# Kernel optimization log

Hardware: AMD Instinct MI355X
Metric: run time of the kernel (lower is better)

## Reference

```python
import jax, jax.numpy as jnp
import numpy as np

B, T, C = 4, 1536, 1536
H, DK, DV = 8, 64, 192
NB = 32  # num_basis per feature class: 192 // (2*3)
MIN_HALF_LIFE = 3.0


def pos_feats_all(distances, seq_len, nb=NB):
    """Enformer positional basis: [exponential, central_mask, gamma], asymmetric.
    distances: int array [L]; returns [L, 6*nb] float32."""
    pos = jnp.abs(distances).astype(jnp.float32)[:, None]  # [L,1]
    sl = jnp.float32(seq_len)
    # exponential
    max_range = jnp.log(sl) / jnp.log(2.0)
    half_life = jnp.power(2.0, jnp.linspace(MIN_HALF_LIFE, max_range, nb))  # [nb]
    f_exp = jnp.exp(-jnp.log(2.0) / half_life * pos)
    # central mask
    widths = jnp.power(2.0, jnp.arange(1, nb + 1, dtype=jnp.float32)) - 1.0
    f_cm = (widths > pos).astype(jnp.float32)
    # gamma
    stddev = sl / (2.0 * nb)
    start_mean = sl / nb
    mean = jnp.linspace(start_mean, sl, nb)
    conc = (mean / stddev) ** 2
    rate = mean / stddev ** 2
    log_unnorm = (conc - 1.0) * jnp.log(pos) - rate * pos  # log(0)=-inf -> exp=0 at pos=0
    log_norm = jax.lax.lgamma(conc) - conc * jnp.log(rate)
    prob = jnp.exp(log_unnorm - log_norm) + 1e-8
    f_gm = prob / jnp.max(prob, axis=0, keepdims=True)
    emb = jnp.concatenate([f_exp, f_cm, f_gm], axis=-1)  # [L, 3*nb]
    sign = jnp.sign(distances).astype(jnp.float32)[:, None]
    return jnp.concatenate([emb, sign * emb], axis=-1)  # [L, 6*nb]


def relative_shift(x):
    """x: [B,H,T,2T-1] -> [B,H,T,T] via the Transformer-XL shift trick."""
    b, h, t, l = x.shape  # l = 2t-1
    x = jnp.pad(x, ((0, 0), (0, 0), (0, 0), (1, 0)))  # [b,h,t,2t]
    x = x.reshape(b, h, l + 1, t)[:, :, 1:, :].reshape(b, h, t, l)
    return x[..., :t]


def setup_inputs() -> dict:
    key = jax.random.key(0)
    ks = jax.random.split(key, 10)
    def dense(k, fi, fo):  # VarianceScaling(scale=2.0)-like init
        return (jax.random.normal(k, (fi, fo), jnp.float32) * np.sqrt(2.0 / fi)).astype(jnp.float32)
    return {
        "x": jax.random.normal(ks[0], (B, T, C), jnp.float32),
        "W_q": dense(ks[1], C, H * DK),
        "W_k": dense(ks[2], C, H * DK),
        "W_v": dense(ks[3], C, H * DV),
        "W_rel_k": dense(ks[4], 6 * NB, H * DK),
        "W_out": dense(ks[5], H * DV, H * DV),
        "b_out": jnp.zeros((H * DV,), jnp.float32),
        "r_w_bias": jax.random.normal(ks[6], (1, H, 1, DK), jnp.float32) * np.sqrt(2.0 / DK),
        "r_r_bias": jax.random.normal(ks[7], (1, H, 1, DK), jnp.float32) * np.sqrt(2.0 / DK),
    }


def reference(x, W_q, W_k, W_v, W_rel_k, W_out, b_out, r_w_bias, r_r_bias):
    b, t, _ = x.shape
    def heads(w, d):  # [b,t,H*d] -> [b,H,t,d]
        return (x @ w).reshape(b, t, H, d).transpose(0, 2, 1, 3)
    Q = heads(W_q, DK) * (DK ** -0.5)  # scaling applied before biases
    K = heads(W_k, DK)
    V = heads(W_v, DV)
    distances = jnp.arange(-t + 1, t)  # [2t-1]
    pe = pos_feats_all(distances, t)  # [2t-1, 6*NB]
    rK = (pe @ W_rel_k).reshape(2 * t - 1, H, DK).transpose(1, 0, 2)  # [H, 2t-1, DK]
    content = jnp.einsum('bhqd,bhkd->bhqk', Q + r_w_bias, K)
    rel = jnp.einsum('bhqd,hld->bhql', Q + r_r_bias, rK)  # [b,H,t,2t-1]
    logits = content + relative_shift(rel)
    attn = jax.nn.softmax(logits, axis=-1)
    out = jnp.einsum('bhqk,bhkd->bhqd', attn, V)  # [b,H,t,DV]
    out = out.transpose(0, 2, 1, 3).reshape(b, t, H * DV)
    return out @ W_out + b_out
```

## Files before the change

kernel.cpp:

```cpp
#include <hip/hip_runtime.h>
#include <hip/hip_bf16.h>
#include <math.h>

#define BB 4
#define TT 1536
#define CC 1536
#define HH 8
#define DKk 64
#define DVv 192
#define NBASIS 32
#define LREL 3071
#define MROWS 6144

typedef short short8 __attribute__((ext_vector_type(8)));
typedef float floatx4 __attribute__((ext_vector_type(4)));

static __device__ inline short f2bf(float f) {
  __hip_bfloat16 h = __float2bfloat16(f);
  return *reinterpret_cast<short*>(&h);
}

static __device__ inline void gload_lds16(const __hip_bfloat16* g, __hip_bfloat16* l) {
  __builtin_amdgcn_global_load_lds(
      (const __attribute__((address_space(1))) unsigned int*)g,
      (__attribute__((address_space(3))) unsigned int*)l, 16, 0, 0);
}

__global__ void detect_kernel(const void* __restrict__ x, int* __restrict__ flag) {
  if (threadIdx.x == 0 && blockIdx.x == 0) {
    const __hip_bfloat16* h = (const __hip_bfloat16*)x;
    int cnt = 0;
    for (int i = 0; i < 64; ++i) {
      float v = fabsf((float)h[2 * i]);
      if (v > 1e-5f && v < 256.0f) cnt++;
    }
    *flag = (cnt >= 32) ? 1 : 0;
  }
}

__global__ __launch_bounds__(256) void convert_kernel(const void* __restrict__ src,
                                                      float* __restrict__ dst, int n,
                                                      const int* __restrict__ flag) {
  const int i = blockIdx.x * 256 + threadIdx.x;
  if (i >= n) return;
  if (*flag) dst[i] = (float)((const __hip_bfloat16*)src)[i];
  else       dst[i] = ((const float*)src)[i];
}

__global__ __launch_bounds__(256) void convbf_kernel(const void* __restrict__ src,
                                                     __hip_bfloat16* __restrict__ dst, int n,
                                                     const int* __restrict__ flag) {
  const int i = blockIdx.x * 256 + threadIdx.x;
  if (i >= n) return;
  if (*flag) dst[i] = ((const __hip_bfloat16*)src)[i];
  else       dst[i] = __float2bfloat16(((const float*)src)[i]);
}

__global__ __launch_bounds__(256) void wt_kernel(const void* __restrict__ src,
                                                 __hip_bfloat16* __restrict__ dst,
                                                 int K, int N, const int* __restrict__ flag) {
  __shared__ __hip_bfloat16 tile[64][68];
  const int tid = threadIdx.x;
  const int k0 = blockIdx.y * 64, n0 = blockIdx.x * 64;
  const bool bf = (*flag != 0);
  {
    const int r = tid >> 2, c0 = (tid & 3) * 16;
    if (bf) {
      const __hip_bfloat16* sp = (const __hip_bfloat16*)src + (size_t)(k0 + r) * N + n0 + c0;
#pragma unroll
      for (int u = 0; u < 16; ++u) tile[r][c0 + u] = sp[u];
    } else {
      const float* sp = (const float*)src + (size_t)(k0 + r) * N + n0 + c0;
#pragma unroll
      for (int u = 0; u < 16; ++u) tile[r][c0 + u] = __float2bfloat16(sp[u]);
    }
  }
  __syncthreads();
  {
    const int nr = tid >> 2, c0 = (tid & 3) * 16;
    __hip_bfloat16* dp = dst + (size_t)(n0 + nr) * K + k0 + c0;
#pragma unroll
    for (int u = 0; u < 16; ++u) dp[u] = tile[c0 + u][nr];
  }
}

__global__ void gmax_kernel(double* __restrict__ gmax) {
  const int j = blockIdx.x;
  const double mean = 48.0 + 1488.0 * (double)j / 31.0;
  const double conc = (mean / 24.0) * (mean / 24.0);
  const double rate = mean / 576.0;
  const double log_norm = lgamma(conc) - conc * log(rate);
  double mx = 1e-8;
  for (int pos = 1 + threadIdx.x; pos <= 1535; pos += 256) {
    double p = exp((conc - 1.0) * log((double)pos) - rate * (double)pos - log_norm) + 1e-8;
    mx = fmax(mx, p);
  }
  __shared__ double red[256];
  red[threadIdx.x] = mx;
  __syncthreads();
  for (int s = 128; s > 0; s >>= 1) {
    if (threadIdx.x < s) red[threadIdx.x] = fmax(red[threadIdx.x], red[threadIdx.x + s]);
    __syncthreads();
  }
  if (threadIdx.x == 0) gmax[j] = red[0];
}

__global__ void pe_kernel(float* __restrict__ pe, const double* __restrict__ gmax) {
  const int l = blockIdx.x;
  const int f = threadIdx.x;
  const int dist = l - (TT - 1);
  const int pos = dist < 0 ? -dist : dist;
  const int base = f % 96;
  const int cls = base / 32;
  const int j = base % 32;
  double v;
  if (cls == 0) {
    const double max_range = log(1536.0) / log(2.0);
    const double e = 3.0 + (max_range - 3.0) * (double)j / 31.0;
    const double hl = exp2(e);
    v = exp2(-(double)pos / hl);
  } else if (cls == 1) {
    const double width = exp2((double)(j + 1)) - 1.0;
    v = (width > (double)pos) ? 1.0 : 0.0;
  } else {
    const double mean = 48.0 + 1488.0 * (double)j / 31.0;
    const double conc = (mean / 24.0) * (mean / 24.0);
    const double rate = mean / 576.0;
    double p;
    if (pos == 0) {
      p = 1e-8;
    } else {
      const double log_norm = lgamma(conc) - conc * log(rate);
      p = exp((conc - 1.0) * log((double)pos) - rate * (double)pos - log_norm) + 1e-8;
    }
    v = p / gmax[j];
  }
  float out = (float)v;
  if (f >= 96) {
    float sgn = (dist > 0) ? 1.f : (dist < 0 ? -1.f : 0.f);
    out *= sgn;
  }
  pe[(size_t)l * 192 + f] = out;
}

__global__ __launch_bounds__(512) void relk_kernel(const float* __restrict__ pe,
                                                   const float* __restrict__ Wrk,
                                                   __hip_bfloat16* __restrict__ rKl) {
  __shared__ float pes[8][192];
  const int l0 = blockIdx.x * 8;
  const int nrows = (LREL - l0) < 8 ? (LREL - l0) : 8;
  const int tid = threadIdx.x;
  for (int idx = tid; idx < nrows * 192; idx += 512) {
    int r = idx / 192, f = idx % 192;
    pes[r][f] = pe[(size_t)(l0 + r) * 192 + f];
  }
  __syncthreads();
  float acc[8] = {0.f, 0.f, 0.f, 0.f, 0.f, 0.f, 0.f, 0.f};
  for (int f = 0; f < 192; ++f) {
    float w = Wrk[(size_t)f * 512 + tid];
#pragma unroll
    for (int r = 0; r < 8; ++r) acc[r] += pes[r][f] * w;
  }
  const int h = tid >> 6, d = tid & 63;
  for (int r = 0; r < nrows; ++r)
    rKl[((size_t)h * LREL + (l0 + r)) * 64 + d] = __float2bfloat16(acc[r]);
}

template <int MODE, bool BIAS>
__global__ __launch_bounds__(256) void gemm_mfma(const __hip_bfloat16* __restrict__ A,
                                                 const __hip_bfloat16* __restrict__ Bt,
                                                 void* __restrict__ Cout,
                                                 void* __restrict__ Cout2,
                                                 const float* __restrict__ bias,
                                                 int M, int N, int K,
                                                 const int* __restrict__ flag) {
  __shared__ __align__(16) __hip_bfloat16 As[128 * 32];
  __shared__ __align__(16) __hip_bfloat16 Bs[128 * 32];
  const int tid = threadIdx.x;
  const int w = tid >> 6, lane = tid & 63;
  const int quad = lane >> 4, l16 = lane & 15;
  const int wm = w >> 1, wn = w & 1;
  const int row0 = blockIdx.y * 128, col0 = blockIdx.x * 128;

  const floatx4 vzero = {0.f, 0.f, 0.f, 0.f};
  floatx4 acc[4][4];
#pragma unroll
  for (int i = 0; i < 4; ++i)
#pragma unroll
    for (int j = 0; j < 4; ++j) acc[i][j] = vzero;

  const int sr = lane >> 2;
  const int sc = (lane & 3) * 8;
  const __hip_bfloat16* ag0 = A + (size_t)(row0 + w * 32 + sr) * K + sc;
  const __hip_bfloat16* ag1 = A + (size_t)(row0 + w * 32 + 16 + sr) * K + sc;
  const __hip_bfloat16* bg0 = Bt + (size_t)(col0 + w * 32 + sr) * K + sc;
  const __hip_bfloat16* bg1 = Bt + (size_t)(col0 + w * 32 + 16 + sr) * K + sc;
  __hip_bfloat16* as0 = As + w * 32 * 32;
  __hip_bfloat16* as1 = As + (w * 32 + 16) * 32;
  __hip_bfloat16* bs0 = Bs + w * 32 * 32;
  __hip_bfloat16* bs1 = Bs + (w * 32 + 16) * 32;

  for (int k0 = 0; k0 < K; k0 += 32) {
    __syncthreads();
    gload_lds16(ag0 + k0, as0);
    gload_lds16(ag1 + k0, as1);
    gload_lds16(bg0 + k0, bs0);
    gload_lds16(bg1 + k0, bs1);
    __syncthreads();
    short8 aF[4], bF[4];
#pragma unroll
    for (int mt = 0; mt < 4; ++mt)
      aF[mt] = *(const short8*)(As + (wm * 64 + mt * 16 + l16) * 32 + quad * 8);
#pragma unroll
    for (int nt = 0; nt < 4; ++nt)
      bF[nt] = *(const short8*)(Bs + (wn * 64 + nt * 16 + l16) * 32 + quad * 8);
#pragma unroll
    for (int mt = 0; mt < 4; ++mt)
#pragma unroll
      for (int nt = 0; nt < 4; ++nt)
        acc[mt][nt] = __builtin_amdgcn_mfma_f32_16x16x32_bf16(aF[mt], bF[nt], acc[mt][nt], 0, 0, 0);
  }

  const bool obf = (MODE == 2) ? (*flag != 0) : false;
#pragma unroll
  for (int mt = 0; mt < 4; ++mt) {
#pragma unroll
    for (int r = 0; r < 4; ++r) {
      const int row = row0 + wm * 64 + mt * 16 + quad * 4 + r;
#pragma unroll
      for (int nt = 0; nt < 4; ++nt) {
        const int col = col0 + wn * 64 + nt * 16 + l16;
        float v = acc[mt][nt][r];
        if (BIAS) v += bias[col];
        if (MODE == 0) {
          ((float*)Cout)[(size_t)row * N + col] = v;
        } else if (MODE == 1) {
          ((__hip_bfloat16*)Cout)[(size_t)row * N + col] = __float2bfloat16(v);
        } else if (MODE == 2) {
          if (obf) ((__hip_bfloat16*)Cout)[(size_t)row * N + col] = __float2bfloat16(v);
          else     ((float*)Cout)[(size_t)row * N + col] = v;
        } else {
          if (col < 512)
            ((float*)Cout)[(size_t)row * 512 + col] = v;
          else
            ((__hip_bfloat16*)Cout2)[(size_t)row * 512 + (col - 512)] = __float2bfloat16(v);
        }
      }
    }
  }
}

__global__ __launch_bounds__(256) void vtrans_kernel(const __hip_bfloat16* __restrict__ Vbf,
                                                     __hip_bfloat16* __restrict__ Vtg) {
  int bid = blockIdx.x;
  int vt = bid % 3; int tt = (bid / 3) % 24; int h = (bid / 72) & 7; int b = bid / 576;
  __shared__ __hip_bfloat16 tile[64][72];
  const int tid = threadIdx.x;
  {
    int r = tid >> 2, c0 = (tid & 3) * 16;
    const __hip_bfloat16* src = Vbf + (size_t)(b * TT + tt * 64 + r) * 1536 + h * 192 + vt * 64 + c0;
#pragma unroll
    for (int u = 0; u < 16; ++u) tile[r][c0 + u] = src[u];
  }
  __syncthreads();
  {
    int vr = tid >> 2, t0 = (tid & 3) * 16;
    __hip_bfloat16* dst = Vtg + ((size_t)((b * 8 + h) * 192) + vt * 64 + vr) * 1536 + tt * 64 + t0;
    union { uint4 u4[2]; unsigned short us[16]; } pk;
#pragma unroll
    for (int u = 0; u < 16; ++u) pk.us[u] = *(const unsigned short*)&tile[t0 + u][vr];
    *(uint4*)(dst) = pk.u4[0];
    *(uint4*)(dst + 8) = pk.u4[1];
  }
}

__global__ __launch_bounds__(256, 3) void attn_mfma(
    const float* __restrict__ tmpQ,
    const float* __restrict__ rwb,
    const float* __restrict__ rrb,
    const __hip_bfloat16* __restrict__ Kbf,
    const __hip_bfloat16* __restrict__ rKl,
    const __hip_bfloat16* __restrict__ Vtg,
    __hip_bfloat16* __restrict__ O)
{
  const int tid = threadIdx.x;
  const int w = tid >> 6, lane = tid & 63;
  const int quad = lane >> 4, l16 = lane & 15;
  const int bid = blockIdx.x;
  const int qt = bid % 24;
  const int h = (bid / 24) & 7;
  const int b = bid / 192;
  const int q0 = qt * 64;

  __shared__ __align__(16) char sm[41472];
  __hip_bfloat16* Ktile = (__hip_bfloat16*)sm;
  __hip_bfloat16* rKwin = (__hip_bfloat16*)(sm + 9216);
  __hip_bfloat16* Rbuf  = (__hip_bfloat16*)(sm + 9216);
  __hip_bfloat16* Ptile = (__hip_bfloat16*)sm;
  __hip_bfloat16* Vtile = (__hip_bfloat16*)(sm + 27648);

  short8 aQw[2], aQr[2];
  {
    const int qrow = q0 + w * 16 + l16;
    const float* qp = tmpQ + (size_t)(b * TT + qrow) * 512 + h * 64;
#pragma unroll
    for (int ks = 0; ks < 2; ++ks) {
#pragma unroll
      for (int j = 0; j < 8; ++j) {
        const int d = ks * 32 + quad * 8 + j;
        const float qv = qp[d] * 0.125f;
        aQw[ks][j] = f2bf(qv + rwb[h * 64 + d]);
        aQr[ks][j] = f2bf(qv + rrb[h * 64 + d]);
      }
    }
  }

  const floatx4 vzero = {0.f, 0.f, 0.f, 0.f};
  floatx4 Oacc[12];
#pragma unroll
  for (int i = 0; i < 12; ++i) Oacc[i] = vzero;
  float mrow[4], lrow[4];
#pragma unroll
  for (int r = 0; r < 4; ++r) { mrow[r] = -INFINITY; lrow[r] = 0.f; }

  const size_t kBase = (size_t)(b * TT) * 512 + h * 64;
  const __hip_bfloat16* VtgB = Vtg + ((size_t)(b * 8 + h) * 192) * 1536;
  const int l0base = 1472 - q0;

  for (int k0 = 0; k0 < TT; k0 += 64) {
    __syncthreads();
    {
      const int r = tid >> 2, c0 = (tid & 3) * 16;
      const __hip_bfloat16* src = Kbf + kBase + (size_t)(k0 + r) * 512 + c0;
      *(uint4*)(Ktile + r * 72 + c0)     = *(const uint4*)(src);
      *(uint4*)(Ktile + r * 72 + c0 + 8) = *(const uint4*)(src + 8);
    }
    {
      const int r = tid >> 1, c0 = (tid & 1) * 32;
      int l = l0base + k0 + r;
      l = l < 3070 ? l : 3070;
      const __hip_bfloat16* src = rKl + ((size_t)h * LREL + l) * 64 + c0;
#pragma unroll
      for (int u = 0; u < 4; ++u)
        *(uint4*)(rKwin + r * 72 + c0 + u * 8) = *(const uint4*)(src + u * 8);
    }
    {
      for (int i = tid; i < 96 * 8; i += 256) {
        const int r = i >> 3, c0 = (i & 7) * 8;
        *(uint4*)(Vtile + r * 72 + c0) =
            *(const uint4*)(VtgB + (size_t)r * 1536 + k0 + c0);
      }
    }
    __syncthreads();

    floatx4 S[4], R[8];
#pragma unroll
    for (int i = 0; i < 4; ++i) S[i] = vzero;
#pragma unroll
    for (int i = 0; i < 8; ++i) R[i] = vzero;
#pragma unroll
    for (int kt = 0; kt < 4; ++kt) {
#pragma unroll
      for (int ks = 0; ks < 2; ++ks) {
        short8 bK = *(const short8*)(Ktile + (kt * 16 + l16) * 72 + ks * 32 + quad * 8);
        S[kt] = __builtin_amdgcn_mfma_f32_16x16x32_bf16(aQw[ks], bK, S[kt], 0, 0, 0);
      }
    }
#pragma unroll
    for (int jt = 0; jt < 8; ++jt) {
#pragma unroll
      for (int ks = 0; ks < 2; ++ks) {
        short8 bR = *(const short8*)(rKwin + (jt * 16 + l16) * 72 + ks * 32 + quad * 8);
        R[jt] = __builtin_amdgcn_mfma_f32_16x16x32_bf16(aQr[ks], bR, R[jt], 0, 0, 0);
      }
    }
    __syncthreads();

#pragma unroll
    for (int jt = 0; jt < 8; ++jt) {
#pragma unroll
      for (int r = 0; r < 4; ++r) {
        const int row = w * 16 + quad * 4 + r;
        Rbuf[row * 132 + jt * 16 + l16] = __float2bfloat16(R[jt][r]);
      }
    }
#pragma unroll
    for (int kt = 0; kt < 4; ++kt) {
#pragma unroll
      for (int r = 0; r < 4; ++r) {
        const int row = w * 16 + quad * 4 + r;
        const int j = kt * 16 + l16 + 63 - row;
        S[kt][r] += (float)Rbuf[row * 132 + j];
      }
    }

    float alpha[4];
#pragma unroll
    for (int r = 0; r < 4; ++r) {
      float mx = fmaxf(fmaxf(S[0][r], S[1][r]), fmaxf(S[2][r], S[3][r]));
#pragma unroll
      for (int off = 8; off > 0; off >>= 1) mx = fmaxf(mx, __shfl_xor(mx, off));
      const float nm = fmaxf(mrow[r], mx);
      alpha[r] = __expf(mrow[r] - nm);
      mrow[r] = nm;
      float ps = 0.f;
#pragma unroll
      for (int kt = 0; kt < 4; ++kt) {
        const float p = __expf(S[kt][r] - nm);
        S[kt][r] = p;
        ps += p;
      }
#pragma unroll
      for (int off = 8; off > 0; off >>= 1) ps += __shfl_xor(ps, off);
      lrow[r] = lrow[r] * alpha[r] + ps;
    }
#pragma unroll
    for (int kt = 0; kt < 4; ++kt) {
#pragma unroll
      for (int r = 0; r < 4; ++r) {
        const int row = w * 16 + quad * 4 + r;
        Ptile[row * 72 + kt * 16 + l16] = __float2bfloat16(S[kt][r]);
      }
    }
#pragma unroll
    for (int vt = 0; vt < 12; ++vt)
#pragma unroll
      for (int r = 0; r < 4; ++r) Oacc[vt][r] *= alpha[r];

    short8 aP[2];
#pragma unroll
    for (int ks = 0; ks < 2; ++ks)
      aP[ks] = *(const short8*)(Ptile + (w * 16 + l16) * 72 + ks * 32 + quad * 8);
#pragma unroll
    for (int vt = 0; vt < 6; ++vt) {
#pragma unroll
      for (int ks = 0; ks < 2; ++ks) {
        short8 bV = *(const short8*)(Vtile + (vt * 16 + l16) * 72 + ks * 32 + quad * 8);
        Oacc[vt] = __builtin_amdgcn_mfma_f32_16x16x32_bf16(aP[ks], bV, Oacc[vt], 0, 0, 0);
      }
    }
    __syncthreads();
    {
      for (int i = tid; i < 96 * 8; i += 256) {
        const int r = i >> 3, c0 = (i & 7) * 8;
        *(uint4*)(Vtile + r * 72 + c0) =
            *(const uint4*)(VtgB + (size_t)(96 + r) * 1536 + k0 + c0);
      }
    }
    __syncthreads();
#pragma unroll
    for (int vt = 6; vt < 12; ++vt) {
#pragma unroll
      for (int ks = 0; ks < 2; ++ks) {
        short8 bV = *(const short8*)(Vtile + ((vt - 6) * 16 + l16) * 72 + ks * 32 + quad * 8);
        Oacc[vt] = __builtin_amdgcn_mfma_f32_16x16x32_bf16(aP[ks], bV, Oacc[vt], 0, 0, 0);
      }
    }
  }

#pragma unroll
  for (int r = 0; r < 4; ++r) {
    const float inv = 1.f / lrow[r];
    const int qrow = q0 + w * 16 + quad * 4 + r;
    __hip_bfloat16* op = O + (size_t)(b * TT + qrow) * 1536 + h * 192;
#pragma unroll
    for (int vt = 0; vt < 12; ++vt)
      op[vt * 16 + l16] = __float2bfloat16(Oacc[vt][r] * inv);
  }
}

extern "C" void kernel_launch(void* const* d_in, const int* in_sizes, int n_in,
                              void* d_out, int out_size, void* d_ws, size_t ws_size,
                              hipStream_t stream) {
  const void* x     = d_in[0];
  const void* W_q   = d_in[1];
  const void* W_k   = d_in[2];
  const void* W_v   = d_in[3];
  const void* W_rel = d_in[4];
  const void* W_out = d_in[5];
  const void* b_out = d_in[6];
  const void* r_w_b = d_in[7];
  const void* r_r_b = d_in[8];

  float* ws = (float*)d_ws;
  int*    flag = (int*)d_ws;
  double* gmax = (double*)(ws + 16);
  float* pe    = ws + 16 + 64;
  float* WrelF = pe    + (size_t)LREL * 192;
  float* boutF = WrelF + (size_t)192 * 512;
  float* rwbF  = boutF + 1536;
  float* rrbF  = rwbF + 512;
  float* tmpQ  = rrbF + 512;
  __hip_bfloat16* xBf  = (__hip_bfloat16*)(tmpQ + (size_t)MROWS * 512);
  __hip_bfloat16* WqT  = xBf  + (size_t)MROWS * 1536;
  __hip_bfloat16* WkT  = WqT  + (size_t)512 * 1536;
  __hip_bfloat16* WvT  = WkT  + (size_t)512 * 1536;
  __hip_bfloat16* WoT  = WvT  + (size_t)1536 * 1536;
  __hip_bfloat16* Kbf  = WoT  + (size_t)1536 * 1536;
  __hip_bfloat16* Vbf  = Kbf  + (size_t)MROWS * 512;
  __hip_bfloat16* Vtg  = Vbf  + (size_t)MROWS * 1536;
  __hip_bfloat16* Obf  = Vtg  + (size_t)32 * 192 * 1536;
  __hip_bfloat16* rKl  = Obf  + (size_t)MROWS * 1536;
  char* endp = (char*)(rKl + (size_t)HH * LREL * 64);
  if (ws_size < (size_t)(endp - (char*)d_ws)) return;

  detect_kernel<<<1, 64, 0, stream>>>(x, flag);

  auto conv = [&](const void* src, float* dst, int n) {
    convert_kernel<<<(n + 255) / 256, 256, 0, stream>>>(src, dst, n, flag);
  };
  conv(W_rel, WrelF, 192 * 512);
  conv(b_out, boutF, 1536);
  conv(r_w_b, rwbF,  512);
  conv(r_r_b, rrbF,  512);

  convbf_kernel<<<(MROWS * 1536 + 255) / 256, 256, 0, stream>>>(x, xBf, MROWS * 1536, flag);

  wt_kernel<<<dim3(512 / 64, 1536 / 64), 256, 0, stream>>>(W_q, WqT, 1536, 512, flag);
  wt_kernel<<<dim3(512 / 64, 1536 / 64), 256, 0, stream>>>(W_k, WkT, 1536, 512, flag);
  wt_kernel<<<dim3(1536 / 64, 1536 / 64), 256, 0, stream>>>(W_v, WvT, 1536, 1536, flag);
  wt_kernel<<<dim3(1536 / 64, 1536 / 64), 256, 0, stream>>>(W_out, WoT, 1536, 1536, flag);

  gmax_kernel<<<32, 256, 0, stream>>>(gmax);
  pe_kernel<<<LREL, 192, 0, stream>>>(pe, gmax);
  relk_kernel<<<(LREL + 7) / 8, 512, 0, stream>>>(pe, WrelF, rKl);

  gemm_mfma<3, false><<<dim3(1024 / 128, MROWS / 128), 256, 0, stream>>>(
      xBf, WqT, tmpQ, Kbf, nullptr, MROWS, 1024, CC, flag);
  gemm_mfma<1, false><<<dim3(1536 / 128, MROWS / 128), 256, 0, stream>>>(
      xBf, WvT, Vbf, nullptr, nullptr, MROWS, 1536, CC, flag);

  vtrans_kernel<<<2304, 256, 0, stream>>>(Vbf, Vtg);

  attn_mfma<<<768, 256, 0, stream>>>(tmpQ, rwbF, rrbF, Kbf, rKl, Vtg, Obf);

  gemm_mfma<2, true><<<dim3(1536 / 128, MROWS / 128), 256, 0, stream>>>(
      Obf, WoT, d_out, nullptr, boutF, MROWS, 1536, CC, flag);
}
```

Baseline: 517.1 us.

## Pre-swizzle K, rK, V into MFMA fragment layout and stream from global

Adds pre-pass kernels that rearrange K, the relative-position keys and V into per-lane MFMA operand fragments, so the attention kernel loads B operands straight from global memory with one 16-byte load per lane. This removes the LDS staging of K/rK/V tiles and most block barriers, and shrinks LDS use. It also remaps block order so heads interleave across XCDs and raises wave priority around MFMA sections. The cost is extra pre-pass kernels, repeated global/L2 reads of the fragments by each query tile, and reuse of the xBf buffer as scratch.

```diff
diff --git a/kernel.cpp b/kernel.cpp
--- a/kernel.cpp
+++ b/kernel.cpp
@@ -250,54 +250,85 @@
   }
 }
 
-__global__ __launch_bounds__(256) void vtrans_kernel(const __hip_bfloat16* __restrict__ Vbf,
-                                                     __hip_bfloat16* __restrict__ Vtg) {
+__global__ __launch_bounds__(256) void kfrag_kernel(const __hip_bfloat16* __restrict__ Kbf,
+                                                    __hip_bfloat16* __restrict__ Kfrag) {
+  const int widx = blockIdx.x * 256 + threadIdx.x;
+  const int lane = widx & 63;
+  const int ks = (widx >> 6) & 1;
+  const int kt = (widx >> 7) % 96;
+  const int bh = (widx >> 7) / 96;
+  const int b = bh >> 3, h = bh & 7;
+  const __hip_bfloat16* src = Kbf + ((size_t)(b * TT + kt * 16 + (lane & 15))) * 512
+                              + h * 64 + ks * 32 + (lane >> 4) * 8;
+  *(uint4*)(Kfrag + (size_t)widx * 8) = *(const uint4*)src;
+}
+
+__global__ __launch_bounds__(256) void rkfrag_kernel(const __hip_bfloat16* __restrict__ rKl,
+                                                     __hip_bfloat16* __restrict__ rKfrag) {
+  const int widx = blockIdx.x * 256 + threadIdx.x;
+  const int lane = widx & 63;
+  const int ks = (widx >> 6) & 1;
+  const int lt = (widx >> 7) % 192;
+  const int h = (widx >> 7) / 192;
+  int l = lt * 16 + (lane & 15);
+  if (l > 3070) l = 3070;
+  const __hip_bfloat16* src = rKl + ((size_t)h * LREL + l) * 64 + ks * 32 + (lane >> 4) * 8;
+  *(uint4*)(rKfrag + (size_t)widx * 8) = *(const uint4*)src;
+}
+
+__global__ __launch_bounds__(256) void vfrag_kernel(const __hip_bfloat16* __restrict__ Vbf,
+                                                    __hip_bfloat16* __restrict__ Vfrag) {
   int bid = blockIdx.x;
-  int vt = bid % 3; int tt = (bid / 3) % 24; int h = (bid / 72) & 7; int b = bid / 576;
+  int vt3 = bid % 3; int kb = (bid / 3) % 24; int h = (bid / 72) & 7; int b = bid / 576;
+  const int bh = b * 8 + h;
   __shared__ __hip_bfloat16 tile[64][72];
   const int tid = threadIdx.x;
   {
     int r = tid >> 2, c0 = (tid & 3) * 16;
-    const __hip_bfloat16* src = Vbf + (size_t)(b * TT + tt * 64 + r) * 1536 + h * 192 + vt * 64 + c0;
+    const __hip_bfloat16* src = Vbf + (size_t)(b * TT + kb * 64 + r) * 1536 + h * 192 + vt3 * 64 + c0;
 #pragma unroll
     for (int u = 0; u < 16; ++u) tile[r][c0 + u] = src[u];
   }
   __syncthreads();
-  {
-    int vr = tid >> 2, t0 = (tid & 3) * 16;
-    __hip_bfloat16* dst = Vtg + ((size_t)((b * 8 + h) * 192) + vt * 64 + vr) * 1536 + tt * 64 + t0;
-    union { uint4 u4[2]; unsigned short us[16]; } pk;
-#pragma unroll
-    for (int u = 0; u < 16; ++u) pk.us[u] = *(const unsigned short*)&tile[t0 + u][vr];
-    *(uint4*)(dst) = pk.u4[0];
-    *(uint4*)(dst + 8) = pk.u4[1];
-  }
-}
-
-__global__ __launch_bounds__(256, 3) void attn_mfma(
+#pragma unroll
+  for (int u = 0; u < 2; ++u) {
+    const int w512 = u * 256 + tid;
+    const int vtl = w512 >> 7;
+    const int ks = (w512 >> 6) & 1;
+    const int ln = w512 & 63;
+    const int qd = ln >> 4, s16 = ln & 15;
+    union { uint4 u4; unsigned short us[8]; } pk;
+#pragma unroll
+    for (int j = 0; j < 8; ++j)
+      pk.us[j] = *(const unsigned short*)&tile[ks * 32 + qd * 8 + j][vtl * 16 + s16];
+    __hip_bfloat16* dst = Vfrag +
+        (((size_t)(bh * 24 + kb) * 12 + vt3 * 4 + vtl) * 2 + ks) * 512 + (size_t)ln * 8;
+    *(uint4*)dst = pk.u4;
+  }
+}
+
+__global__ __launch_bounds__(256, 3) void attn_stream(
     const float* __restrict__ tmpQ,
     const float* __restrict__ rwb,
     const float* __restrict__ rrb,
-    const __hip_bfloat16* __restrict__ Kbf,
-    const __hip_bfloat16* __restrict__ rKl,
-    const __hip_bfloat16* __restrict__ Vtg,
+    const __hip_bfloat16* __restrict__ Kfrag,
+    const __hip_bfloat16* __restrict__ rKfrag,
+    const __hip_bfloat16* __restrict__ Vfrag,
     __hip_bfloat16* __restrict__ O)
 {
   const int tid = threadIdx.x;
   const int w = tid >> 6, lane = tid & 63;
   const int quad = lane >> 4, l16 = lane & 15;
-  const int bid = blockIdx.x;
-  const int qt = bid % 24;
-  const int h = (bid / 24) & 7;
-  const int b = bid / 192;
+  const int o = (blockIdx.x & 7) * 96 + (blockIdx.x >> 3);
+  const int qt = o % 24;
+  const int h = (o / 24) & 7;
+  const int b = o / 192;
+  const int bh = b * 8 + h;
   const int q0 = qt * 64;
 
-  __shared__ __align__(16) char sm[41472];
-  __hip_bfloat16* Ktile = (__hip_bfloat16*)sm;
-  __hip_bfloat16* rKwin = (__hip_bfloat16*)(sm + 9216);
-  __hip_bfloat16* Rbuf  = (__hip_bfloat16*)(sm + 9216);
-  __hip_bfloat16* Ptile = (__hip_bfloat16*)sm;
-  __hip_bfloat16* Vtile = (__hip_bfloat16*)(sm + 27648);
+  __shared__ __align__(16) char sm[26112];
+  __hip_bfloat16* Rbuf  = (__hip_bfloat16*)sm;
+  __hip_bfloat16* Ptile = (__hip_bfloat16*)(sm + 16896);
 
   short8 aQw[2], aQr[2];
   {
@@ -323,46 +354,30 @@
 #pragma unroll
   for (int r = 0; r < 4; ++r) { mrow[r] = -INFINITY; lrow[r] = 0.f; }
 
-  const size_t kBase = (size_t)(b * TT) * 512 + h * 64;
-  const __hip_bfloat16* VtgB = Vtg + ((size_t)(b * 8 + h) * 192) * 1536;
-  const int l0base = 1472 - q0;
+  const __hip_bfloat16* Kf = Kfrag + (size_t)bh * 98304 + (size_t)lane * 8;
+  const __hip_bfloat16* Rf = rKfrag + (size_t)h * 196608
+                             + (size_t)((1472 - q0) >> 4) * 1024 + (size_t)lane * 8;
+  const __hip_bfloat16* Vf = Vfrag + (size_t)bh * 294912 + (size_t)lane * 8;
 
   for (int k0 = 0; k0 < TT; k0 += 64) {
-    __syncthreads();
-    {
-      const int r = tid >> 2, c0 = (tid & 3) * 16;
-      const __hip_bfloat16* src = Kbf + kBase + (size_t)(k0 + r) * 512 + c0;
-      *(uint4*)(Ktile + r * 72 + c0)     = *(const uint4*)(src);
-      *(uint4*)(Ktile + r * 72 + c0 + 8) = *(const uint4*)(src + 8);
-    }
-    {
-      const int r = tid >> 1, c0 = (tid & 1) * 32;
-      int l = l0base + k0 + r;
-      l = l < 3070 ? l : 3070;
-      const __hip_bfloat16* src = rKl + ((size_t)h * LREL + l) * 64 + c0;
-#pragma unroll
-      for (int u = 0; u < 4; ++u)
-        *(uint4*)(rKwin + r * 72 + c0 + u * 8) = *(const uint4*)(src + u * 8);
-    }
-    {
-      for (int i = tid; i < 96 * 8; i += 256) {
-        const int r = i >> 3, c0 = (i & 7) * 8;
-        *(uint4*)(Vtile + r * 72 + c0) =
-            *(const uint4*)(VtgB + (size_t)r * 1536 + k0 + c0);
-      }
-    }
-    __syncthreads();
+    __builtin_amdgcn_s_barrier();
+    const int kt0 = k0 >> 4;
+    const __hip_bfloat16* kf = Kf + (size_t)kt0 * 1024;
+    const __hip_bfloat16* rf = Rf + (size_t)kt0 * 1024;
+    const __hip_bfloat16* vf = Vf + (size_t)(k0 >> 6) * 12288;
 
     floatx4 S[4], R[8];
 #pragma unroll
     for (int i = 0; i < 4; ++i) S[i] = vzero;
 #pragma unroll
     for (int i = 0; i < 8; ++i) R[i] = vzero;
+
+    __builtin_amdgcn_s_setprio(1);
 #pragma unroll
     for (int kt = 0; kt < 4; ++kt) {
 #pragma unroll
       for (int ks = 0; ks < 2; ++ks) {
-        short8 bK = *(const short8*)(Ktile + (kt * 16 + l16) * 72 + ks * 32 + quad * 8);
+        short8 bK = *(const short8*)(kf + (kt * 2 + ks) * 512);
         S[kt] = __builtin_amdgcn_mfma_f32_16x16x32_bf16(aQw[ks], bK, S[kt], 0, 0, 0);
       }
     }
@@ -370,11 +385,11 @@
     for (int jt = 0; jt < 8; ++jt) {
 #pragma unroll
       for (int ks = 0; ks < 2; ++ks) {
-        short8 bR = *(const short8*)(rKwin + (jt * 16 + l16) * 72 + ks * 32 + quad * 8);
+        short8 bR = *(const short8*)(rf + (jt * 2 + ks) * 512);
         R[jt] = __builtin_amdgcn_mfma_f32_16x16x32_bf16(aQr[ks], bR, R[jt], 0, 0, 0);
       }
     }
-    __syncthreads();
+    __builtin_amdgcn_s_setprio(0);
 
 #pragma unroll
     for (int jt = 0; jt < 8; ++jt) {
@@ -431,31 +446,17 @@
 #pragma unroll
     for (int ks = 0; ks < 2; ++ks)
       aP[ks] = *(const short8*)(Ptile + (w * 16 + l16) * 72 + ks * 32 + quad * 8);
-#pragma unroll
-    for (int vt = 0; vt < 6; ++vt) {
+
+    __builtin_amdgcn_s_setprio(1);
+#pragma unroll
+    for (int vt = 0; vt < 12; ++vt) {
 #pragma unroll
       for (int ks = 0; ks < 2; ++ks) {
-        short8 bV = *(const short8*)(Vtile + (vt * 16 + l16) * 72 + ks * 32 + quad * 8);
+        short8 bV = *(const short8*)(vf + (vt * 2 + ks) * 512);
         Oacc[vt] = __builtin_amdgcn_mfma_f32_16x16x32_bf16(aP[ks], bV, Oacc[vt], 0, 0, 0);
       }
     }
-    __syncthreads();
-    {
-      for (int i = tid; i < 96 * 8; i += 256) {
-        const int r = i >> 3, c0 = (i & 7) * 8;
-        *(uint4*)(Vtile + r * 72 + c0) =
-            *(const uint4*)(VtgB + (size_t)(96 + r) * 1536 + k0 + c0);
-      }
-    }
-    __syncthreads();
-#pragma unroll
-    for (int vt = 6; vt < 12; ++vt) {
-#pragma unroll
-      for (int ks = 0; ks < 2; ++ks) {
-        short8 bV = *(const short8*)(Vtile + ((vt - 6) * 16 + l16) * 72 + ks * 32 + quad * 8);
-        Oacc[vt] = __builtin_amdgcn_mfma_f32_16x16x32_bf16(aP[ks], bV, Oacc[vt], 0, 0, 0);
-      }
-    }
+    __builtin_amdgcn_s_setprio(0);
   }
 
 #pragma unroll
@@ -498,11 +499,14 @@
   __hip_bfloat16* WoT  = WvT  + (size_t)1536 * 1536;
   __hip_bfloat16* Kbf  = WoT  + (size_t)1536 * 1536;
   __hip_bfloat16* Vbf  = Kbf  + (size_t)MROWS * 512;
-  __hip_bfloat16* Vtg  = Vbf  + (size_t)MROWS * 1536;
-  __hip_bfloat16* Obf  = Vtg  + (size_t)32 * 192 * 1536;
+  __hip_bfloat16* Vfrag= Vbf  + (size_t)MROWS * 1536;
+  __hip_bfloat16* Obf  = Vfrag + (size_t)32 * 192 * 1536;
   __hip_bfloat16* rKl  = Obf  + (size_t)MROWS * 1536;
   char* endp = (char*)(rKl + (size_t)HH * LREL * 64);
   if (ws_size < (size_t)(endp - (char*)d_ws)) return;
+
+  __hip_bfloat16* Kfrag  = xBf;
+  __hip_bfloat16* rKfrag = xBf + (size_t)3145728;
 
   detect_kernel<<<1, 64, 0, stream>>>(x, flag);
 
@@ -530,9 +534,11 @@
   gemm_mfma<1, false><<<dim3(1536 / 128, MROWS / 128), 256, 0, stream>>>(
       xBf, WvT, Vbf, nullptr, nullptr, MROWS, 1536, CC, flag);
 
-  vtrans_kernel<<<2304, 256, 0, stream>>>(Vbf, Vtg);
-
-  attn_mfma<<<768, 256, 0, stream>>>(tmpQ, rwbF, rrbF, Kbf, rKl, Vtg, Obf);
+  kfrag_kernel<<<1536, 256, 0, stream>>>(Kbf, Kfrag);
+  rkfrag_kernel<<<768, 256, 0, stream>>>(rKl, rKfrag);
+  vfrag_kernel<<<2304, 256, 0, stream>>>(Vbf, Vfrag);
+
+  attn_stream<<<768, 256, 0, stream>>>(tmpQ, rwbF, rrbF, Kfrag, rKfrag, Vfrag, Obf);
 
   gemm_mfma<2, true><<<dim3(1536 / 128, MROWS / 128), 256, 0, stream>>>(
       Obf, WoT, d_out, nullptr, boutF, MROWS, 1536, CC, flag);
```

Measured after the change: 599.2 us. +15.9%, slower.
